# Kernel optimization log

Measured on AMD Instinct MI355X. Metric: run time of the kernel, lower is better.

The kernel has to match this reference:

```python
import jax, jax.numpy as jnp
import numpy as np
from functools import partial

V, MAXS, D, L, H, F = 50257, 1024, 1024, 6, 16, 4096
B, S = 2, 1024
DK = D // H
EPS = 1e-5


def _layer_norm(x, g, b):
    mu = jnp.mean(x, axis=-1, keepdims=True)
    var = jnp.mean(jnp.square(x - mu), axis=-1, keepdims=True)
    return (x - mu) * jax.lax.rsqrt(var + EPS) * g + b


def _rotate_half(x):
    x1, x2 = x[..., : x.shape[-1] // 2], x[..., x.shape[-1] // 2 :]
    return jnp.concatenate([-x2, x1], axis=-1)


def setup_inputs() -> dict:
    key = jax.random.key(0)
    ks = jax.random.split(key, 10)
    std = 0.02
    inp = {
        'input_ids': jax.random.randint(ks[0], (B, S), 0, V),
        'tok_emb': jax.random.normal(ks[1], (V, D), jnp.float32) * std,
        'pos_emb': jax.random.normal(ks[2], (MAXS, D), jnp.float32) * std,
        'wq': jax.random.normal(ks[3], (L, D, D), jnp.float32) * std,
        'wk': jax.random.normal(ks[4], (L, D, D), jnp.float32) * std,
        'wv': jax.random.normal(ks[5], (L, D, D), jnp.float32) * std,
        'wo': jax.random.normal(ks[6], (L, D, D), jnp.float32) * std,
        'w1': jax.random.normal(ks[7], (L, F, D), jnp.float32) * std,
        'w2': jax.random.normal(ks[8], (L, D, F), jnp.float32) * std,
        'w3': jax.random.normal(ks[9], (L, F, D), jnp.float32) * std,
        'ln1_g': jnp.ones((L, D), jnp.float32),
        'ln1_b': jnp.zeros((L, D), jnp.float32),
        'ln2_g': jnp.ones((L, D), jnp.float32),
        'ln2_b': jnp.zeros((L, D), jnp.float32),
        'lnf_g': jnp.ones((D,), jnp.float32),
        'lnf_b': jnp.zeros((D,), jnp.float32),
    }
    return inp


def reference(input_ids, tok_emb, pos_emb, wq, wk, wv, wo, w1, w2, w3,
              ln1_g, ln1_b, ln2_g, ln2_b, lnf_g, lnf_b):
    b, s = input_ids.shape
    # embeddings
    x = tok_emb[input_ids] + pos_emb[:s]  # [B,S,D]

    # RoPE cos/sin cache (per-head dim DK)
    inv_freq = 1.0 / (10000.0 ** (jnp.arange(0, DK, 2, dtype=jnp.float32) / DK))
    t = jnp.arange(s, dtype=jnp.float32)
    freqs = t[:, None] * inv_freq[None, :]            # [S,DK/2]
    emb = jnp.concatenate([freqs, freqs], axis=-1)     # [S,DK]
    cos, sin = jnp.cos(emb), jnp.sin(emb)

    causal = jnp.tril(jnp.ones((s, s), dtype=bool))
    scale = 1.0 / np.sqrt(DK)

    def block(xc, p):
        h = _layer_norm(xc, p['ln1_g'], p['ln1_b'])
        # torch Linear: y = x @ W.T, W is [out,in]
        q = jnp.einsum('bsd,od->bso', h, p['wq']).reshape(b, s, H, DK).transpose(0, 2, 1, 3)
        k = jnp.einsum('bsd,od->bso', h, p['wk']).reshape(b, s, H, DK).transpose(0, 2, 1, 3)
        v = jnp.einsum('bsd,od->bso', h, p['wv']).reshape(b, s, H, DK).transpose(0, 2, 1, 3)
        q = q * cos + _rotate_half(q) * sin
        k = k * cos + _rotate_half(k) * sin
        scores = jnp.einsum('bhqd,bhkd->bhqk', q, k) * scale
        scores = jnp.where(causal, scores, -1e9)
        attn = jax.nn.softmax(scores, axis=-1)
        ctx = jnp.einsum('bhqk,bhkd->bhqd', attn, v)
        ctx = ctx.transpose(0, 2, 1, 3).reshape(b, s, D)
        xc = xc + jnp.einsum('bsd,od->bso', ctx, p['wo'])
        h2 = _layer_norm(xc, p['ln2_g'], p['ln2_b'])
        ff = jnp.einsum('bsf,df->bsd',
                        jax.nn.silu(jnp.einsum('bsd,fd->bsf', h2, p['w1']))
                        * jnp.einsum('bsd,fd->bsf', h2, p['w3']),
                        p['w2'])
        xc = xc + ff
        return xc, None

    params = {'wq': wq, 'wk': wk, 'wv': wv, 'wo': wo,
              'w1': w1, 'w2': w2, 'w3': w3,
              'ln1_g': ln1_g, 'ln1_b': ln1_b, 'ln2_g': ln2_g, 'ln2_b': ln2_b}
    x, _ = jax.lax.scan(block, x, params)
    x = _layer_norm(x, lnf_g, lnf_b)
    # attention_mask is None -> return last token representation
    return x[:, -1]
```

## Files before the change

### kernel.cpp

```cpp
#include <hip/hip_runtime.h>
#include <hip/hip_bf16.h>

#define D_ 1024
#define S_ 1024
#define B_ 2
#define H_ 16
#define F_ 4096
#define L_ 6

typedef __bf16 bf16x8 __attribute__((ext_vector_type(8)));
typedef float f32x4 __attribute__((ext_vector_type(4)));

__device__ __forceinline__ unsigned short f2bf(float f){
  union { float f; unsigned u; } v; v.f = f;
  unsigned r = v.u + 0x7fffu + ((v.u >> 16) & 1u);
  return (unsigned short)(r >> 16);
}
__device__ __forceinline__ float bf2f(ushort u){
  union { unsigned u; float f; } v; v.u = ((unsigned)u) << 16; return v.f;
}
__device__ __forceinline__ uint pk2(float lo, float hi){
  return (uint)f2bf(lo) | ((uint)f2bf(hi) << 16);
}
__device__ __forceinline__ uint4 pack8(float4 a, float4 b){
  uint4 r; r.x = pk2(a.x,a.y); r.y = pk2(a.z,a.w); r.z = pk2(b.x,b.y); r.w = pk2(b.z,b.w); return r;
}

__global__ void k_embed(const int* __restrict__ ids, const float* __restrict__ tok,
                        const float* __restrict__ pos, float* __restrict__ x){
  int row = blockIdx.x;
  int s = row & (S_-1);
  int id = ids[row];
  int t = threadIdx.x;
  float4 te = ((const float4*)(tok + (size_t)id*D_))[t];
  float4 pe = ((const float4*)(pos + (size_t)s*D_))[t];
  float4 o; o.x=te.x+pe.x; o.y=te.y+pe.y; o.z=te.z+pe.z; o.w=te.w+pe.w;
  ((float4*)(x + (size_t)row*D_))[t] = o;
}

__global__ void k_ln(const float* __restrict__ x, const float* __restrict__ g,
                     const float* __restrict__ b, ushort* __restrict__ h){
  int row = blockIdx.x;
  int t = threadIdx.x;
  float4 v = ((const float4*)(x + (size_t)row*D_))[t];
  float s1 = v.x+v.y+v.z+v.w;
  float s2 = v.x*v.x+v.y*v.y+v.z*v.z+v.w*v.w;
  #pragma unroll
  for (int o=1;o<64;o<<=1){ s1 += __shfl_xor(s1,o); s2 += __shfl_xor(s2,o); }
  __shared__ float sm[8];
  int w = t>>6;
  if ((t&63)==0){ sm[w]=s1; sm[4+w]=s2; }
  __syncthreads();
  s1 = sm[0]+sm[1]+sm[2]+sm[3];
  s2 = sm[4]+sm[5]+sm[6]+sm[7];
  float mu = s1 * (1.0f/D_);
  float var = s2 * (1.0f/D_) - mu*mu;
  float rs = rsqrtf(var + 1e-5f);
  float4 gv = ((const float4*)g)[t];
  float4 bv = ((const float4*)b)[t];
  union { ushort u[4]; uint2 p; } o;
  o.u[0] = f2bf((v.x-mu)*rs*gv.x + bv.x);
  o.u[1] = f2bf((v.y-mu)*rs*gv.y + bv.y);
  o.u[2] = f2bf((v.z-mu)*rs*gv.z + bv.z);
  o.u[3] = f2bf((v.w-mu)*rs*gv.w + bv.w);
  ((uint2*)(h + (size_t)row*D_))[t] = o.p;
}

__global__ void k_lnf(const float* __restrict__ xf, const float* __restrict__ g,
                      const float* __restrict__ b, float* __restrict__ out){
  int row = blockIdx.x;
  int t = threadIdx.x;
  float4 v = ((const float4*)(xf + (size_t)row*D_))[t];
  float s1 = v.x+v.y+v.z+v.w;
  float s2 = v.x*v.x+v.y*v.y+v.z*v.z+v.w*v.w;
  #pragma unroll
  for (int o=1;o<64;o<<=1){ s1 += __shfl_xor(s1,o); s2 += __shfl_xor(s2,o); }
  __shared__ float sm[8];
  int w = t>>6;
  if ((t&63)==0){ sm[w]=s1; sm[4+w]=s2; }
  __syncthreads();
  s1 = sm[0]+sm[1]+sm[2]+sm[3];
  s2 = sm[4]+sm[5]+sm[6]+sm[7];
  float mu = s1 * (1.0f/D_);
  float var = s2 * (1.0f/D_) - mu*mu;
  float rs = rsqrtf(var + 1e-5f);
  float4 gv = ((const float4*)g)[t];
  float4 bv = ((const float4*)b)[t];
  float4 y;
  y.x = (v.x-mu)*rs*gv.x + bv.x;
  y.y = (v.y-mu)*rs*gv.y + bv.y;
  y.z = (v.z-mu)*rs*gv.z + bv.z;
  y.w = (v.w-mu)*rs*gv.w + bv.w;
  ((float4*)(out + (size_t)row*D_))[t] = y;
}

#define LDA 40
template<int OP>
__global__ __launch_bounds__(256) void k_gemm_bt(
    const ushort* __restrict__ A,
    const float* __restrict__ B0, const float* __restrict__ B1, const float* __restrict__ B2,
    float* __restrict__ C0, float* __restrict__ C1, float* __restrict__ C2,
    int N, int K, int kchunks, int coff){
  const int z = blockIdx.z;
  const int mat = z / kchunks, chunk = z - mat*kchunks;
  const float* B = (mat==0) ? B0 : ((mat==1) ? B1 : B2);
  float* C = (mat==0) ? C0 : ((mat==1) ? C1 : C2);
  if (OP == 0) C += (size_t)chunk * coff;
  const int Kc = K / kchunks;
  const int kbeg = chunk*Kc, kend = kbeg + Kc;
  const int m0 = blockIdx.x*128, n0 = blockIdx.y*128;
  __shared__ ushort As[128*LDA];
  __shared__ ushort Bs[128*LDA];
  const int t = threadIdx.x;
  const int lane = t & 63, w = t >> 6;
  const int wm = (w & 1)*64, wn = (w >> 1)*64;
  const int fr = lane & 15, fk = (lane >> 4)*8;
  const int trow = t >> 1, tcol = (t & 1)*16;
  const ushort* Ag = A + (size_t)(m0 + trow)*K + tcol;
  const float*  Bg = B + (size_t)(n0 + trow)*K + tcol;
  ushort* Asw = &As[trow*LDA + tcol];
  ushort* Bsw = &Bs[trow*LDA + tcol];

  f32x4 acc[4][4];
  #pragma unroll
  for (int i=0;i<4;i++)
    #pragma unroll
    for (int j=0;j<4;j++)
      #pragma unroll
      for (int r=0;r<4;r++) acc[i][j][r] = 0.0f;

  for (int k0 = kbeg; k0 < kend; k0 += 32){
    uint4 a0 = *(const uint4*)(Ag + k0);
    uint4 a1 = *(const uint4*)(Ag + k0 + 8);
    float4 q0 = *(const float4*)(Bg + k0);
    float4 q1 = *(const float4*)(Bg + k0 + 4);
    float4 q2 = *(const float4*)(Bg + k0 + 8);
    float4 q3 = *(const float4*)(Bg + k0 + 12);
    __syncthreads();
    *(uint4*)(Asw)     = a0;
    *(uint4*)(Asw + 8) = a1;
    *(uint4*)(Bsw)     = pack8(q0, q1);
    *(uint4*)(Bsw + 8) = pack8(q2, q3);
    __syncthreads();
    bf16x8 af[4], bfr[4];
    #pragma unroll
    for (int i=0;i<4;i++) af[i]  = *(const bf16x8*)&As[(wm + i*16 + fr)*LDA + fk];
    #pragma unroll
    for (int j=0;j<4;j++) bfr[j] = *(const bf16x8*)&Bs[(wn + j*16 + fr)*LDA + fk];
    #pragma unroll
    for (int i=0;i<4;i++)
      #pragma unroll
      for (int j=0;j<4;j++)
        acc[i][j] = __builtin_amdgcn_mfma_f32_16x16x32_bf16(af[i], bfr[j], acc[i][j], 0, 0, 0);
  }
  #pragma unroll
  for (int i=0;i<4;i++){
    int row = m0 + wm + i*16 + (lane >> 4)*4;
    #pragma unroll
    for (int j=0;j<4;j++){
      int col = n0 + wn + j*16 + (lane & 15);
      float* cp = C + (size_t)row*N + col;
      #pragma unroll
      for (int r=0;r<4;r++){
        if (OP == 0) cp[(size_t)r*N] = acc[i][j][r];
        else         atomicAdd(cp + (size_t)r*N, acc[i][j][r]);
      }
    }
  }
}

__global__ __launch_bounds__(256) void k_gemm_w13(
    const ushort* __restrict__ A,
    const float* __restrict__ W1, const float* __restrict__ W3,
    ushort* __restrict__ P){
  const int m0 = blockIdx.x*128, n0 = blockIdx.y*64;
  __shared__ ushort As [128*LDA];
  __shared__ ushort B1s[64*LDA];
  __shared__ ushort B3s[64*LDA];
  const int t = threadIdx.x;
  const int lane = t & 63, w = t >> 6;
  const int wm = (w & 1)*64, wn = (w >> 1)*32;
  const int fr = lane & 15, fk = (lane >> 4)*8;
  const int trA = t >> 1, tcA = (t & 1)*16;
  const int trB = t >> 2, tcB = (t & 3)*8;
  const ushort* Ag  = A  + (size_t)(m0 + trA)*D_ + tcA;
  const float*  B1g = W1 + (size_t)(n0 + trB)*D_ + tcB;
  const float*  B3g = W3 + (size_t)(n0 + trB)*D_ + tcB;
  ushort* Asw = &As [trA*LDA + tcA];
  ushort* B1w = &B1s[trB*LDA + tcB];
  ushort* B3w = &B3s[trB*LDA + tcB];

  f32x4 a1[4][2], a3[4][2];
  #pragma unroll
  for (int i=0;i<4;i++)
    #pragma unroll
    for (int j=0;j<2;j++)
      #pragma unroll
      for (int r=0;r<4;r++){ a1[i][j][r]=0.f; a3[i][j][r]=0.f; }

  for (int k0 = 0; k0 < D_; k0 += 32){
    uint4 av0 = *(const uint4*)(Ag + k0);
    uint4 av1 = *(const uint4*)(Ag + k0 + 8);
    float4 p0 = *(const float4*)(B1g + k0);
    float4 p1 = *(const float4*)(B1g + k0 + 4);
    float4 r0 = *(const float4*)(B3g + k0);
    float4 r1 = *(const float4*)(B3g + k0 + 4);
    __syncthreads();
    *(uint4*)(Asw)     = av0;
    *(uint4*)(Asw + 8) = av1;
    *(uint4*)(B1w)     = pack8(p0, p1);
    *(uint4*)(B3w)     = pack8(r0, r1);
    __syncthreads();
    bf16x8 af[4], b1f[2], b3f[2];
    #pragma unroll
    for (int i=0;i<4;i++) af[i]  = *(const bf16x8*)&As [(wm + i*16 + fr)*LDA + fk];
    #pragma unroll
    for (int j=0;j<2;j++){
      b1f[j] = *(const bf16x8*)&B1s[(wn + j*16 + fr)*LDA + fk];
      b3f[j] = *(const bf16x8*)&B3s[(wn + j*16 + fr)*LDA + fk];
    }
    #pragma unroll
    for (int i=0;i<4;i++)
      #pragma unroll
      for (int j=0;j<2;j++){
        a1[i][j] = __builtin_amdgcn_mfma_f32_16x16x32_bf16(af[i], b1f[j], a1[i][j], 0, 0, 0);
        a3[i][j] = __builtin_amdgcn_mfma_f32_16x16x32_bf16(af[i], b3f[j], a3[i][j], 0, 0, 0);
      }
  }
  #pragma unroll
  for (int i=0;i<4;i++){
    int row = m0 + wm + i*16 + (lane >> 4)*4;
    #pragma unroll
    for (int j=0;j<2;j++){
      int col = n0 + wn + j*16 + (lane & 15);
      #pragma unroll
      for (int r=0;r<4;r++){
        float u = a1[i][j][r];
        float s = u / (1.f + expf(-u)) * a3[i][j][r];
        P[(size_t)(row + r)*F_ + col] = f2bf(s);
      }
    }
  }
}

__global__ void k_prep(const float* __restrict__ q0, const float* __restrict__ q1,
                       const float* __restrict__ kp0, const float* __restrict__ kp1,
                       const float* __restrict__ v0, const float* __restrict__ v1,
                       ushort* __restrict__ qdst, ushort* __restrict__ kdst,
                       ushort* __restrict__ vt, int mode){
  __shared__ float vl[64*68];
  const int half = (B_*S_*D_)/256;
  int bx = blockIdx.x;
  int t = threadIdx.x;
  const int nrope = (mode == 0) ? 2*half : half;
  if (bx < nrope){
    const float *src0, *src1; ushort* dst;
    if (mode == 0 && bx < half){ src0 = q0; src1 = q1; dst = qdst; }
    else { src0 = kp0; src1 = kp1; dst = kdst; if (mode == 0) bx -= half; }
    int idx = bx*256 + t;
    int d = idx & 63;
    int s = (idx >> 10) & (S_-1);
    float v = src0[idx] + src1[idx];
    float p = __shfl_xor(v, 32);
    float rot = (d < 32) ? -p : p;
    float inv = expf(-(float)(d & 31) * 0.28782313662f);
    float sn, cs; sincosf((float)s * inv, &sn, &cs);
    dst[idx] = f2bf(v*cs + rot*sn);
    return;
  }
  bx -= nrope;
  int s0 = (bx & 15)*64, bh = bx >> 4;
  int b = bh >> 4, hh = bh & 15;
  int j = t >> 2, off = (t & 3)*16;
  size_t sidx = ((size_t)(b*S_ + s0 + j))*D_ + hh*64 + off;
  const float* sa = v0 + sidx;
  const float* sb = v1 + sidx;
  #pragma unroll
  for (int q=0; q<4; q++){
    float4 ra = ((const float4*)sa)[q];
    float4 rb = ((const float4*)sb)[q];
    float4 rs; rs.x=ra.x+rb.x; rs.y=ra.y+rb.y; rs.z=ra.z+rb.z; rs.w=ra.w+rb.w;
    *(float4*)&vl[j*68 + off + q*4] = rs;
  }
  __syncthreads();
  int d = t >> 2, so = (t & 3)*16;
  ushort* dst = vt + ((size_t)bh*64 + d)*S_ + s0 + so;
  union { ushort u[8]; uint4 q; } o0, o1;
  #pragma unroll
  for (int jj=0; jj<8; jj++) o0.u[jj] = f2bf(vl[(so + jj)*68 + d]);
  #pragma unroll
  for (int jj=0; jj<8; jj++) o1.u[jj] = f2bf(vl[(so + 8 + jj)*68 + d]);
  *(uint4*)dst       = o0.q;
  *(uint4*)(dst + 8) = o1.q;
}

#define LDK 72
__global__ __launch_bounds__(256) void k_flash(
    const ushort* __restrict__ qh, const ushort* __restrict__ kh,
    const ushort* __restrict__ vt, ushort* __restrict__ ctx){
  __shared__ ushort Kl[64*LDK];
  __shared__ ushort Vl[64*LDK];
  __shared__ ushort Pl[4][16*LDK];
  const int t = threadIdx.x, lane = t & 63, w = t >> 6;
  const int bh = blockIdx.x, b = bh >> 4, hh = bh & 15;
  const int yy = blockIdx.y;
  const int q0 = 64 * ((yy < 8) ? (15 - 2*yy) : (2*yy - 16));
  const int qw = q0 + w*16;
  const int fr = lane & 15, fk = (lane >> 4)*8;
  bf16x8 qf0, qf1;
  {
    const ushort* qp = qh + ((size_t)(b*S_ + qw + fr))*D_ + hh*64;
    qf0 = *(const bf16x8*)(qp + fk);
    qf1 = *(const bf16x8*)(qp + 32 + fk);
  }
  f32x4 o[4];
  float m[4], l[4];
  #pragma unroll
  for (int r=0;r<4;r++){
    m[r] = -1e30f; l[r] = 0.f;
    #pragma unroll
    for (int j=0;j<4;j++) o[j][r] = 0.f;
  }
  const int nch = q0/64 + 1;
  const int sr = t >> 2, soff = (t & 3)*16;
  ushort* Plw = Pl[w];
  const int rbase = qw + (lane >> 4)*4;
  for (int c=0; c<nch; c++){
    const int k0 = c*64;
    __syncthreads();
    {
      const uint4* ks = (const uint4*)(kh + ((size_t)(b*S_ + k0 + sr))*D_ + hh*64 + soff);
      uint4 ka = ks[0], kb2 = ks[1];
      const uint4* vs = (const uint4*)(vt + ((size_t)(bh*64 + sr))*S_ + k0 + soff);
      uint4 va = vs[0], vb2 = vs[1];
      *(uint4*)&Kl[sr*LDK + soff]     = ka;
      *(uint4*)&Kl[sr*LDK + soff + 8] = kb2;
      *(uint4*)&Vl[sr*LDK + soff]     = va;
      *(uint4*)&Vl[sr*LDK + soff + 8] = vb2;
    }
    __syncthreads();
    f32x4 sc[4];
    #pragma unroll
    for (int j=0;j<4;j++){
      bf16x8 kf0 = *(const bf16x8*)&Kl[(j*16 + fr)*LDK + fk];
      bf16x8 kf1 = *(const bf16x8*)&Kl[(j*16 + fr)*LDK + 32 + fk];
      f32x4 z; z[0]=0.f; z[1]=0.f; z[2]=0.f; z[3]=0.f;
      z = __builtin_amdgcn_mfma_f32_16x16x32_bf16(qf0, kf0, z, 0, 0, 0);
      sc[j] = __builtin_amdgcn_mfma_f32_16x16x32_bf16(qf1, kf1, z, 0, 0, 0);
    }
    #pragma unroll
    for (int r=0;r<4;r++){
      const int qrow = rbase + r;
      float mc = -1e30f;
      #pragma unroll
      for (int j=0;j<4;j++){
        float sv = (k0 + j*16 + fr <= qrow) ? sc[j][r]*0.125f : -1e30f;
        sc[j][r] = sv;
        mc = fmaxf(mc, sv);
      }
      #pragma unroll
      for (int ofs=1; ofs<16; ofs<<=1) mc = fmaxf(mc, __shfl_xor(mc, ofs));
      float mn = fmaxf(m[r], mc);
      float al = expf(m[r] - mn);
      float sum = 0.f;
      #pragma unroll
      for (int j=0;j<4;j++){
        float p = expf(sc[j][r] - mn);
        sum += p;
        Plw[(((lane >> 4)*4) + r)*LDK + j*16 + fr] = f2bf(p);
      }
      #pragma unroll
      for (int ofs=1; ofs<16; ofs<<=1) sum += __shfl_xor(sum, ofs);
      l[r] = l[r]*al + sum;
      m[r] = mn;
      #pragma unroll
      for (int j=0;j<4;j++) o[j][r] *= al;
    }
    bf16x8 pa0 = *(const bf16x8*)&Plw[fr*LDK + fk];
    bf16x8 pa1 = *(const bf16x8*)&Plw[fr*LDK + 32 + fk];
    #pragma unroll
    for (int j=0;j<4;j++){
      bf16x8 vf0 = *(const bf16x8*)&Vl[(j*16 + fr)*LDK + fk];
      bf16x8 vf1 = *(const bf16x8*)&Vl[(j*16 + fr)*LDK + 32 + fk];
      o[j] = __builtin_amdgcn_mfma_f32_16x16x32_bf16(pa0, vf0, o[j], 0, 0, 0);
      o[j] = __builtin_amdgcn_mfma_f32_16x16x32_bf16(pa1, vf1, o[j], 0, 0, 0);
    }
  }
  #pragma unroll
  for (int r=0;r<4;r++){
    float rl = 1.0f / l[r];
    ushort* cp = ctx + ((size_t)(b*S_ + rbase + r))*D_ + hh*64 + fr;
    #pragma unroll
    for (int j=0;j<4;j++) cp[j*16] = f2bf(o[j][r] * rl);
  }
}

__global__ __launch_bounds__(256) void k_row1(
    const ushort* __restrict__ A0, const ushort* __restrict__ A1,
    const float* __restrict__ B, int K,
    const float* __restrict__ add0, const float* __restrict__ add1,
    float* __restrict__ C, int N){
  __shared__ ushort As[2*4096];
  const int t = threadIdx.x;
  const int nv = 2*K/8;
  for (int i = t; i < nv; i += 256){
    int row = (i*8 >= K) ? 1 : 0;
    int off = i*8 - row*K;
    ((uint4*)As)[i] = *(const uint4*)((row ? A1 : A0) + off);
  }
  __syncthreads();
  const int col = blockIdx.x*16 + (t >> 4);
  const int p = t & 15;
  const float* Bp = B + (size_t)col*K;
  float acc0 = 0.f, acc1 = 0.f;
  for (int i = 0; i < K/64; i++){
    int k = p*4 + i*64;
    float4 bv = *(const float4*)(Bp + k);
    ushort4 u0 = *(const ushort4*)&As[k];
    ushort4 u1 = *(const ushort4*)&As[K + k];
    acc0 += bv.x*bf2f(u0.x) + bv.y*bf2f(u0.y) + bv.z*bf2f(u0.z) + bv.w*bf2f(u0.w);
    acc1 += bv.x*bf2f(u1.x) + bv.y*bf2f(u1.y) + bv.z*bf2f(u1.z) + bv.w*bf2f(u1.w);
  }
  #pragma unroll
  for (int ofs=1; ofs<16; ofs<<=1){ acc0 += __shfl_xor(acc0, ofs); acc1 += __shfl_xor(acc1, ofs); }
  if (p == 0){
    C[col]     = (add0 ? add0[col] : 0.f) + acc0;
    C[N + col] = (add1 ? add1[col] : 0.f) + acc1;
  }
}

__global__ __launch_bounds__(256) void k_row13(
    const ushort* __restrict__ H2,
    const float* __restrict__ W1, const float* __restrict__ W3,
    ushort* __restrict__ P){
  __shared__ ushort As[2*1024];
  const int t = threadIdx.x;
  ((uint4*)As)[t] = *(const uint4*)(H2 + t*8);
  __syncthreads();
  const int col = blockIdx.x*16 + (t >> 4);
  const int p = t & 15;
  const float* b1 = W1 + (size_t)col*D_;
  const float* b3 = W3 + (size_t)col*D_;
  float u10=0.f, u11=0.f, u30=0.f, u31=0.f;
  for (int i = 0; i < D_/64; i++){
    int k = p*4 + i*64;
    float4 v1 = *(const float4*)(b1 + k);
    float4 v3 = *(const float4*)(b3 + k);
    ushort4 a0 = *(const ushort4*)&As[k];
    ushort4 a1 = *(const ushort4*)&As[D_ + k];
    float f00=bf2f(a0.x), f01=bf2f(a0.y), f02=bf2f(a0.z), f03=bf2f(a0.w);
    float f10=bf2f(a1.x), f11=bf2f(a1.y), f12=bf2f(a1.z), f13=bf2f(a1.w);
    u10 += v1.x*f00 + v1.y*f01 + v1.z*f02 + v1.w*f03;
    u11 += v1.x*f10 + v1.y*f11 + v1.z*f12 + v1.w*f13;
    u30 += v3.x*f00 + v3.y*f01 + v3.z*f02 + v3.w*f03;
    u31 += v3.x*f10 + v3.y*f11 + v3.z*f12 + v3.w*f13;
  }
  #pragma unroll
  for (int ofs=1; ofs<16; ofs<<=1){
    u10 += __shfl_xor(u10, ofs); u11 += __shfl_xor(u11, ofs);
    u30 += __shfl_xor(u30, ofs); u31 += __shfl_xor(u31, ofs);
  }
  if (p == 0){
    P[col]      = f2bf(u10 / (1.f + expf(-u10)) * u30);
    P[F_ + col] = f2bf(u11 / (1.f + expf(-u11)) * u31);
  }
}

__global__ __launch_bounds__(256) void k_dec(
    const float* __restrict__ q2,
    const ushort* __restrict__ kh,
    const ushort* __restrict__ vt,
    ushort* __restrict__ c2){
  __shared__ float qs[64];
  __shared__ float ps[S_];
  __shared__ float red[8];
  const int t = threadIdx.x, lane = t & 63, w = t >> 6;
  const int bh = blockIdx.x, b = bh >> 4, hh = bh & 15;
  if (t < 64){
    int d = t;
    float v = q2[b*D_ + hh*64 + d];
    float pr = q2[b*D_ + hh*64 + (d ^ 32)];
    float rot = (d < 32) ? -pr : pr;
    float inv = expf(-(float)(d & 31) * 0.28782313662f);
    float sn, cs; sincosf((float)(S_-1) * inv, &sn, &cs);
    qs[d] = v*cs + rot*sn;
  }
  __syncthreads();
  float sc[4];
  #pragma unroll
  for (int j=0;j<4;j++){
    int key = t + j*256;
    const uint4* kp = (const uint4*)(kh + ((size_t)(b*S_ + key))*D_ + hh*64);
    float acc = 0.f;
    #pragma unroll
    for (int i=0;i<8;i++){
      uint4 kv = kp[i];
      const ushort* ku = (const ushort*)&kv;
      #pragma unroll
      for (int jj=0;jj<8;jj++) acc += qs[i*8+jj] * bf2f(ku[jj]);
    }
    sc[j] = acc * 0.125f;
  }
  float mx = fmaxf(fmaxf(sc[0],sc[1]), fmaxf(sc[2],sc[3]));
  #pragma unroll
  for (int ofs=1; ofs<64; ofs<<=1) mx = fmaxf(mx, __shfl_xor(mx, ofs));
  if (lane == 0) red[w] = mx;
  __syncthreads();
  mx = fmaxf(fmaxf(red[0],red[1]), fmaxf(red[2],red[3]));
  float ls = 0.f;
  #pragma unroll
  for (int j=0;j<4;j++){
    float pv = expf(sc[j] - mx);
    ps[t + j*256] = pv;
    ls += pv;
  }
  #pragma unroll
  for (int ofs=1; ofs<64; ofs<<=1) ls += __shfl_xor(ls, ofs);
  if (lane == 0) red[4 + w] = ls;
  __syncthreads();
  const float L = red[4]+red[5]+red[6]+red[7];
  const int d = t >> 2, part = t & 3;
  const uint4* vp = (const uint4*)(vt + ((size_t)(bh*64 + d))*S_ + part*256);
  float acc = 0.f;
  for (int i=0;i<32;i++){
    uint4 vv = vp[i];
    const ushort* vu = (const ushort*)&vv;
    #pragma unroll
    for (int jj=0;jj<8;jj++) acc += ps[part*256 + i*8 + jj] * bf2f(vu[jj]);
  }
  acc += __shfl_xor(acc, 1);
  acc += __shfl_xor(acc, 2);
  if (part == 0) c2[b*D_ + hh*64 + d] = f2bf(acc / L);
}

extern "C" void kernel_launch(void* const* d_in, const int* in_sizes, int n_in,
                              void* d_out, int out_size, void* d_ws, size_t ws_size,
                              hipStream_t stream) {
  const int*   ids  = (const int*)  d_in[0];
  const float* tok  = (const float*)d_in[1];
  const float* pos  = (const float*)d_in[2];
  const float* wq   = (const float*)d_in[3];
  const float* wk   = (const float*)d_in[4];
  const float* wv   = (const float*)d_in[5];
  const float* wo   = (const float*)d_in[6];
  const float* w1   = (const float*)d_in[7];
  const float* w2   = (const float*)d_in[8];
  const float* w3   = (const float*)d_in[9];
  const float* ln1g = (const float*)d_in[10];
  const float* ln1b = (const float*)d_in[11];
  const float* ln2g = (const float*)d_in[12];
  const float* ln2b = (const float*)d_in[13];
  const float* lnfg = (const float*)d_in[14];
  const float* lnfb = (const float*)d_in[15];

  char* wsb = (char*)d_ws;
  float*  x  = (float*) (wsb);
  ushort* h  = (ushort*)(wsb + (size_t)8*1024*1024);
  ushort* vt = (ushort*)(wsb + (size_t)12*1024*1024);
  ushort* qh = (ushort*)(wsb + (size_t)16*1024*1024);
  ushort* kh = (ushort*)(wsb + (size_t)20*1024*1024);
  ushort* cx = (ushort*)(wsb + (size_t)24*1024*1024);
  float*  q2 = (float*) (wsb + (size_t)28*1024*1024);
  ushort* c2 = (ushort*)(wsb + (size_t)28*1024*1024 + 8192);
  float*  xl = (float*) (wsb + (size_t)28*1024*1024 + 16384);
  ushort* h2 = (ushort*)(wsb + (size_t)28*1024*1024 + 24576);
  ushort* pl = (ushort*)(wsb + (size_t)28*1024*1024 + 32768);
  float*  xf = (float*) (wsb + (size_t)28*1024*1024 + 49152);
  float*  qp = (float*) (wsb + (size_t)48*1024*1024);
  ushort* pb = (ushort*)(wsb + (size_t)112*1024*1024);

  const int QKV_COFF = 8*1024*1024;
  float* kp = qp + 2*1024*1024;
  float* vp = qp + 4*1024*1024;

  k_embed<<<B_*S_, 256, 0, stream>>>(ids, tok, pos, x);

  for (int l = 0; l < L_; l++){
    size_t od = (size_t)l*D_*D_;
    size_t fd = (size_t)l*F_*D_;
    if (l < L_-1){
      k_ln<<<B_*S_, 256, 0, stream>>>(x, ln1g + l*D_, ln1b + l*D_, h);
      k_gemm_bt<0><<<dim3(16, 8, 6), 256, 0, stream>>>(h, wq + od, wk + od, wv + od,
                                                       qp, kp, vp, D_, D_, 2, QKV_COFF);
      k_prep<<<2*(B_*S_*D_)/256 + (S_/64)*B_*H_, 256, 0, stream>>>(
          qp, qp + QKV_COFF, kp, kp + QKV_COFF, vp, vp + QKV_COFF, qh, kh, vt, 0);
      k_flash<<<dim3(B_*H_, S_/64), 256, 0, stream>>>(qh, kh, vt, cx);
      k_gemm_bt<1><<<dim3(16, 8, 4), 256, 0, stream>>>(cx, wo + od, nullptr, nullptr,
                                                       x, nullptr, nullptr, D_, D_, 4, 0);
      k_ln<<<B_*S_, 256, 0, stream>>>(x, ln2g + l*D_, ln2b + l*D_, h);
      k_gemm_w13<<<dim3(16, 64), 256, 0, stream>>>(h, w1 + fd, w3 + fd, pb);
      k_gemm_bt<1><<<dim3(16, 8, 8), 256, 0, stream>>>(pb, w2 + fd, nullptr, nullptr,
                                                       x, nullptr, nullptr, D_, F_, 8, 0);
    } else {
      k_ln<<<B_*S_, 256, 0, stream>>>(x, ln1g + l*D_, ln1b + l*D_, h);
      k_gemm_bt<0><<<dim3(16, 8, 4), 256, 0, stream>>>(h, wk + od, wv + od, nullptr,
                                                       kp, vp, nullptr, D_, D_, 2, QKV_COFF);
      k_prep<<<(B_*S_*D_)/256 + (S_/64)*B_*H_, 256, 0, stream>>>(
          nullptr, nullptr, kp, kp + QKV_COFF, vp, vp + QKV_COFF, qh, kh, vt, 1);
      k_row1<<<64, 256, 0, stream>>>(h + (size_t)(S_-1)*D_, h + (size_t)(B_*S_-1)*D_,
                                     wq + od, D_, nullptr, nullptr, q2, D_);
      k_dec<<<B_*H_, 256, 0, stream>>>(q2, kh, vt, c2);
      k_row1<<<64, 256, 0, stream>>>(c2, c2 + D_, wo + od, D_,
                                     x + (size_t)(S_-1)*D_, x + (size_t)(B_*S_-1)*D_, xl, D_);
      k_ln<<<2, 256, 0, stream>>>(xl, ln2g + l*D_, ln2b + l*D_, h2);
      k_row13<<<F_/16, 256, 0, stream>>>(h2, w1 + fd, w3 + fd, pl);
      k_row1<<<64, 256, 0, stream>>>(pl, pl + F_, w2 + fd, F_, xl, xl + D_, xf, D_);
    }
  }

  k_lnf<<<B_, 256, 0, stream>>>(xf, lnfg, lnfb, (float*)d_out);
}
```

Before: 2.078 ms.

## Replace split-K atomics with partial buffers reduced inside fused residual+LayerNorm

The Wo and W2 split-K GEMMs used to atomically add their partial sums straight into the residual stream. They now store plain partials to scratch buffers. A new kernel sums those partials into the residual and applies the next LayerNorm in the same pass, which removes the separate LN launches and the atomic traffic. expf is also swapped for __expf in softmax and SiLU. The cost is extra partial-buffer memory traffic (up to 8 chunks of 8MB), in exchange for no atomics, and the fast exp slightly reduces accuracy.

```diff
diff --git a/kernel.cpp b/kernel.cpp
--- a/kernel.cpp
+++ b/kernel.cpp
@@ -66,6 +66,40 @@
   ((uint2*)(h + (size_t)row*D_))[t] = o.p;
 }
 
+__global__ void k_red_ln(const float* __restrict__ part, int nchunks, int coff,
+                         float* __restrict__ x, const float* __restrict__ g,
+                         const float* __restrict__ b, ushort* __restrict__ h){
+  int row = blockIdx.x;
+  int t = threadIdx.x;
+  float4 v = ((const float4*)(x + (size_t)row*D_))[t];
+  for (int c = 0; c < nchunks; c++){
+    float4 p = ((const float4*)(part + (size_t)c*coff + (size_t)row*D_))[t];
+    v.x += p.x; v.y += p.y; v.z += p.z; v.w += p.w;
+  }
+  ((float4*)(x + (size_t)row*D_))[t] = v;
+  float s1 = v.x+v.y+v.z+v.w;
+  float s2 = v.x*v.x+v.y*v.y+v.z*v.z+v.w*v.w;
+  #pragma unroll
+  for (int o=1;o<64;o<<=1){ s1 += __shfl_xor(s1,o); s2 += __shfl_xor(s2,o); }
+  __shared__ float sm[8];
+  int w = t>>6;
+  if ((t&63)==0){ sm[w]=s1; sm[4+w]=s2; }
+  __syncthreads();
+  s1 = sm[0]+sm[1]+sm[2]+sm[3];
+  s2 = sm[4]+sm[5]+sm[6]+sm[7];
+  float mu = s1 * (1.0f/D_);
+  float var = s2 * (1.0f/D_) - mu*mu;
+  float rs = rsqrtf(var + 1e-5f);
+  float4 gv = ((const float4*)g)[t];
+  float4 bv = ((const float4*)b)[t];
+  union { ushort u[4]; uint2 p; } o;
+  o.u[0] = f2bf((v.x-mu)*rs*gv.x + bv.x);
+  o.u[1] = f2bf((v.y-mu)*rs*gv.y + bv.y);
+  o.u[2] = f2bf((v.z-mu)*rs*gv.z + bv.z);
+  o.u[3] = f2bf((v.w-mu)*rs*gv.w + bv.w);
+  ((uint2*)(h + (size_t)row*D_))[t] = o.p;
+}
+
 __global__ void k_lnf(const float* __restrict__ xf, const float* __restrict__ g,
                       const float* __restrict__ b, float* __restrict__ out){
   int row = blockIdx.x;
@@ -95,7 +129,6 @@
 }
 
 #define LDA 40
-template<int OP>
 __global__ __launch_bounds__(256) void k_gemm_bt(
     const ushort* __restrict__ A,
     const float* __restrict__ B0, const float* __restrict__ B1, const float* __restrict__ B2,
@@ -104,8 +137,7 @@
   const int z = blockIdx.z;
   const int mat = z / kchunks, chunk = z - mat*kchunks;
   const float* B = (mat==0) ? B0 : ((mat==1) ? B1 : B2);
-  float* C = (mat==0) ? C0 : ((mat==1) ? C1 : C2);
-  if (OP == 0) C += (size_t)chunk * coff;
+  float* C = ((mat==0) ? C0 : ((mat==1) ? C1 : C2)) + (size_t)chunk * coff;
   const int Kc = K / kchunks;
   const int kbeg = chunk*Kc, kend = kbeg + Kc;
   const int m0 = blockIdx.x*128, n0 = blockIdx.y*128;
@@ -161,10 +193,7 @@
       int col = n0 + wn + j*16 + (lane & 15);
       float* cp = C + (size_t)row*N + col;
       #pragma unroll
-      for (int r=0;r<4;r++){
-        if (OP == 0) cp[(size_t)r*N] = acc[i][j][r];
-        else         atomicAdd(cp + (size_t)r*N, acc[i][j][r]);
-      }
+      for (int r=0;r<4;r++) cp[(size_t)r*N] = acc[i][j][r];
     }
   }
 }
@@ -236,7 +265,7 @@
       #pragma unroll
       for (int r=0;r<4;r++){
         float u = a1[i][j][r];
-        float s = u / (1.f + expf(-u)) * a3[i][j][r];
+        float s = u / (1.f + __expf(-u)) * a3[i][j][r];
         P[(size_t)(row + r)*F_ + col] = f2bf(s);
       }
     }
@@ -361,11 +390,11 @@
       #pragma unroll
       for (int ofs=1; ofs<16; ofs<<=1) mc = fmaxf(mc, __shfl_xor(mc, ofs));
       float mn = fmaxf(m[r], mc);
-      float al = expf(m[r] - mn);
+      float al = __expf(m[r] - mn);
       float sum = 0.f;
       #pragma unroll
       for (int j=0;j<4;j++){
-        float p = expf(sc[j][r] - mn);
+        float p = __expf(sc[j][r] - mn);
         sum += p;
         Plw[(((lane >> 4)*4) + r)*LDK + j*16 + fr] = f2bf(p);
       }
@@ -461,8 +490,8 @@
     u30 += __shfl_xor(u30, ofs); u31 += __shfl_xor(u31, ofs);
   }
   if (p == 0){
-    P[col]      = f2bf(u10 / (1.f + expf(-u10)) * u30);
-    P[F_ + col] = f2bf(u11 / (1.f + expf(-u11)) * u31);
+    P[col]      = f2bf(u10 / (1.f + __expf(-u10)) * u30);
+    P[F_ + col] = f2bf(u11 / (1.f + __expf(-u11)) * u31);
   }
 }
 
@@ -510,7 +539,7 @@
   float ls = 0.f;
   #pragma unroll
   for (int j=0;j<4;j++){
-    float pv = expf(sc[j] - mx);
+    float pv = __expf(sc[j] - mx);
     ps[t + j*256] = pv;
     ls += pv;
   }
@@ -570,42 +599,46 @@
   ushort* pb = (ushort*)(wsb + (size_t)112*1024*1024);
 
   const int QKV_COFF = 8*1024*1024;
+  const int RED_COFF = 2*1024*1024;
   float* kp = qp + 2*1024*1024;
   float* vp = qp + 4*1024*1024;
 
   k_embed<<<B_*S_, 256, 0, stream>>>(ids, tok, pos, x);
-
-  for (int l = 0; l < L_; l++){
+  k_ln<<<B_*S_, 256, 0, stream>>>(x, ln1g, ln1b, h);
+
+  for (int l = 0; l < L_-1; l++){
     size_t od = (size_t)l*D_*D_;
     size_t fd = (size_t)l*F_*D_;
-    if (l < L_-1){
-      k_ln<<<B_*S_, 256, 0, stream>>>(x, ln1g + l*D_, ln1b + l*D_, h);
-      k_gemm_bt<0><<<dim3(16, 8, 6), 256, 0, stream>>>(h, wq + od, wk + od, wv + od,
-                                                       qp, kp, vp, D_, D_, 2, QKV_COFF);
-      k_prep<<<2*(B_*S_*D_)/256 + (S_/64)*B_*H_, 256, 0, stream>>>(
-          qp, qp + QKV_COFF, kp, kp + QKV_COFF, vp, vp + QKV_COFF, qh, kh, vt, 0);
-      k_flash<<<dim3(B_*H_, S_/64), 256, 0, stream>>>(qh, kh, vt, cx);
-      k_gemm_bt<1><<<dim3(16, 8, 4), 256, 0, stream>>>(cx, wo + od, nullptr, nullptr,
-                                                       x, nullptr, nullptr, D_, D_, 4, 0);
-      k_ln<<<B_*S_, 256, 0, stream>>>(x, ln2g + l*D_, ln2b + l*D_, h);
-      k_gemm_w13<<<dim3(16, 64), 256, 0, stream>>>(h, w1 + fd, w3 + fd, pb);
-      k_gemm_bt<1><<<dim3(16, 8, 8), 256, 0, stream>>>(pb, w2 + fd, nullptr, nullptr,
-                                                       x, nullptr, nullptr, D_, F_, 8, 0);
-    } else {
-      k_ln<<<B_*S_, 256, 0, stream>>>(x, ln1g + l*D_, ln1b + l*D_, h);
-      k_gemm_bt<0><<<dim3(16, 8, 4), 256, 0, stream>>>(h, wk + od, wv + od, nullptr,
-                                                       kp, vp, nullptr, D_, D_, 2, QKV_COFF);
-      k_prep<<<(B_*S_*D_)/256 + (S_/64)*B_*H_, 256, 0, stream>>>(
-          nullptr, nullptr, kp, kp + QKV_COFF, vp, vp + QKV_COFF, qh, kh, vt, 1);
-      k_row1<<<64, 256, 0, stream>>>(h + (size_t)(S_-1)*D_, h + (size_t)(B_*S_-1)*D_,
-                                     wq + od, D_, nullptr, nullptr, q2, D_);
-      k_dec<<<B_*H_, 256, 0, stream>>>(q2, kh, vt, c2);
-      k_row1<<<64, 256, 0, stream>>>(c2, c2 + D_, wo + od, D_,
-                                     x + (size_t)(S_-1)*D_, x + (size_t)(B_*S_-1)*D_, xl, D_);
-      k_ln<<<2, 256, 0, stream>>>(xl, ln2g + l*D_, ln2b + l*D_, h2);
-      k_row13<<<F_/16, 256, 0, stream>>>(h2, w1 + fd, w3 + fd, pl);
-      k_row1<<<64, 256, 0, stream>>>(pl, pl + F_, w2 + fd, F_, xl, xl + D_, xf, D_);
-    }
+    k_gemm_bt<<<dim3(16, 8, 6), 256, 0, stream>>>(h, wq + od, wk + od, wv + od,
+                                                  qp, kp, vp, D_, D_, 2, QKV_COFF);
+    k_prep<<<2*(B_*S_*D_)/256 + (S_/64)*B_*H_, 256, 0, stream>>>(
+        qp, qp + QKV_COFF, kp, kp + QKV_COFF, vp, vp + QKV_COFF, qh, kh, vt, 0);
+    k_flash<<<dim3(B_*H_, S_/64), 256, 0, stream>>>(qh, kh, vt, cx);
+    k_gemm_bt<<<dim3(16, 8, 4), 256, 0, stream>>>(cx, wo + od, nullptr, nullptr,
+                                                  qp, nullptr, nullptr, D_, D_, 4, RED_COFF);
+    k_red_ln<<<B_*S_, 256, 0, stream>>>(qp, 4, RED_COFF, x, ln2g + l*D_, ln2b + l*D_, h);
+    k_gemm_w13<<<dim3(16, 64), 256, 0, stream>>>(h, w1 + fd, w3 + fd, pb);
+    k_gemm_bt<<<dim3(16, 8, 8), 256, 0, stream>>>(pb, w2 + fd, nullptr, nullptr,
+                                                  qp, nullptr, nullptr, D_, F_, 8, RED_COFF);
+    k_red_ln<<<B_*S_, 256, 0, stream>>>(qp, 8, RED_COFF, x, ln1g + (l+1)*D_, ln1b + (l+1)*D_, h);
+  }
+
+  {
+    int l = L_-1;
+    size_t od = (size_t)l*D_*D_;
+    size_t fd = (size_t)l*F_*D_;
+    k_gemm_bt<<<dim3(16, 8, 4), 256, 0, stream>>>(h, wk + od, wv + od, nullptr,
+                                                  kp, vp, nullptr, D_, D_, 2, QKV_COFF);
+    k_prep<<<(B_*S_*D_)/256 + (S_/64)*B_*H_, 256, 0, stream>>>(
+        nullptr, nullptr, kp, kp + QKV_COFF, vp, vp + QKV_COFF, qh, kh, vt, 1);
+    k_row1<<<64, 256, 0, stream>>>(h + (size_t)(S_-1)*D_, h + (size_t)(B_*S_-1)*D_,
+                                   wq + od, D_, nullptr, nullptr, q2, D_);
+    k_dec<<<B_*H_, 256, 0, stream>>>(q2, kh, vt, c2);
+    k_row1<<<64, 256, 0, stream>>>(c2, c2 + D_, wo + od, D_,
+                                   x + (size_t)(S_-1)*D_, x + (size_t)(B_*S_-1)*D_, xl, D_);
+    k_ln<<<2, 256, 0, stream>>>(xl, ln2g + l*D_, ln2b + l*D_, h2);
+    k_row13<<<F_/16, 256, 0, stream>>>(h2, w1 + fd, w3 + fd, pl);
+    k_row1<<<64, 256, 0, stream>>>(pl, pl + F_, w2 + fd, F_, xl, xl + D_, xf, D_);
   }
 
   k_lnf<<<B_, 256, 0, stream>>>(xf, lnfg, lnfb, (float*)d_out);
```

After: 1.801 ms. 13.3% less time.
